# Optimization experiments

Measured on AMD Instinct MI355X. Metric: run time of the kernel, lower is better.

Reference implementation:

```python
import jax, jax.numpy as jnp
import numpy as np

S, N, E = 12, 16384, 262144        # timesteps, nodes, edges per timestep
DIN = DOUT = H = 128               # gcn in/out dim == lstm hidden (required by module)
B = 64                             # batch_size; N % B == 0


def setup_inputs() -> dict:
    key = jax.random.key(0)
    ks = jax.random.split(key, 10)
    return {
        "adj_indices": jax.random.randint(ks[0], (S, 2, E), 0, N, dtype=jnp.int32),
        "adj_values": jax.random.uniform(ks[1], (S, E), dtype=jnp.float32),
        "xs": jax.random.normal(ks[2], (S, N, DIN), dtype=jnp.float32),
        "gcn_weight": jax.random.normal(ks[3], (DIN, DOUT), dtype=jnp.float32) * 0.05,
        "gcn_bias": jnp.zeros((DOUT,), jnp.float32),
        "w_ih": jax.random.normal(ks[4], (4 * H, DOUT), dtype=jnp.float32) * 0.05,
        "w_hh": jax.random.normal(ks[5], (4 * H, H), dtype=jnp.float32) * 0.05,
        "b_ih": jnp.zeros((4 * H,), jnp.float32),
        "b_hh": jnp.zeros((4 * H,), jnp.float32),
        "h0": jax.random.normal(ks[6], (B, H), dtype=jnp.float32),
        "c0": jax.random.normal(ks[7], (B, H), dtype=jnp.float32),
    }


def reference(adj_indices, adj_values, xs, gcn_weight, gcn_bias,
              w_ih, w_hh, b_ih, b_hh, h0, c0):
    # --- GCN per timestep: relu(sparse_A @ (X @ W) + b) ---
    def gcn(idx, vals, x):
        support = x @ gcn_weight                      # [N, DOUT]
        msg = vals[:, None] * support[idx[1]]         # gather cols -> [E, DOUT]
        out = jax.ops.segment_sum(msg, idx[0], num_segments=N)  # scatter rows
        return jax.nn.relu(out + gcn_bias)

    cur = jax.vmap(gcn)(adj_indices, adj_values, xs)  # [S, N, DOUT]
    seq = cur.reshape(-1, B, DOUT)                    # [T=S*N/B, B, H]

    # --- single-layer LSTM (torch gate order: i, f, g, o) ---
    def step(carry, x_t):
        h, c = carry
        gates = x_t @ w_ih.T + b_ih + h @ w_hh.T + b_hh   # [B, 4H]
        i, f, g, o = jnp.split(gates, 4, axis=-1)
        c = jax.nn.sigmoid(f) * c + jax.nn.sigmoid(i) * jnp.tanh(g)
        h = jax.nn.sigmoid(o) * jnp.tanh(c)
        return (h, c), h

    _, hs = jax.lax.scan(step, (h0, c0), seq)         # [T, B, H]
    return hs
```

## Files before the change

kernel.cpp:

```cpp
#include <hip/hip_runtime.h>
#include <cstdint>
#include <cstddef>

#define SS 12
#define NN 16384
#define EE 262144
#define TT 3072

typedef _Float16 h2_t __attribute__((ext_vector_type(2)));
typedef _Float16 f16x8 __attribute__((ext_vector_type(8)));
typedef short bf16x8 __attribute__((ext_vector_type(8)));
typedef float floatx4 __attribute__((ext_vector_type(4)));
typedef unsigned short ushortx8 __attribute__((ext_vector_type(8)));

__device__ __forceinline__ float fast_sig(float x) {
    float e = __builtin_amdgcn_exp2f(-1.442695041f * x);
    return __builtin_amdgcn_rcpf(1.f + e);
}
__device__ __forceinline__ float fast_tanh(float x) {
    float e = __builtin_amdgcn_exp2f(2.885390082f * x);
    return 1.f - 2.f * __builtin_amdgcn_rcpf(e + 1.f);
}
__device__ __forceinline__ unsigned short f2bf(float f) {
    unsigned int x = __float_as_uint(f);
    unsigned int r = (x + 0x7FFFu + ((x >> 16) & 1u)) >> 16;
    return (unsigned short)r;
}
__device__ __forceinline__ float bf2f(unsigned short u) {
    return __uint_as_float(((unsigned int)u) << 16);
}

__global__ void k_zero(int* __restrict__ p) {
    p[blockIdx.x * 256 + threadIdx.x] = 0;
}

__global__ void k_count(const int* __restrict__ adj, int* __restrict__ counts) {
    int i = blockIdx.x * 256 + threadIdx.x;
    int t = i / EE, e = i - t * EE;
    int dst = adj[(size_t)t * 2 * EE + e];
    atomicAdd(&counts[t * NN + dst], 1);
}

__global__ void k_scan(const int* __restrict__ counts, int* __restrict__ offs,
                       int* __restrict__ cursor) {
    __shared__ int sums[1024];
    int t = blockIdx.x, tid = threadIdx.x;
    const int per = NN / 1024;
    int base = t * NN + tid * per;
    int local[16];
    int s = 0;
#pragma unroll
    for (int i = 0; i < per; i++) { local[i] = counts[base + i]; s += local[i]; }
    sums[tid] = s;
    __syncthreads();
    for (int off = 1; off < 1024; off <<= 1) {
        int v = (tid >= off) ? sums[tid - off] : 0;
        __syncthreads();
        sums[tid] += v;
        __syncthreads();
    }
    int run = sums[tid] - s;
#pragma unroll
    for (int i = 0; i < per; i++) { offs[base + i] = run; cursor[base + i] = run; run += local[i]; }
}

__global__ void k_scatter(const int* __restrict__ adj, const float* __restrict__ vals,
                          int* __restrict__ cursor, int2* __restrict__ edges) {
    int i = blockIdx.x * 256 + threadIdx.x;
    int t = i / EE, e = i - t * EE;
    int dst = adj[(size_t)t * 2 * EE + e];
    int src = adj[(size_t)t * 2 * EE + EE + e];
    float v = vals[(size_t)t * EE + e];
    int p = atomicAdd(&cursor[t * NN + dst], 1);
    edges[(size_t)t * EE + p] = make_int2(src, __float_as_int(v));
}

__global__ __launch_bounds__(256) void k_support(const float* __restrict__ xs,
                                                 const float* __restrict__ W,
                                                 unsigned short* __restrict__ sup) {
    __shared__ float Ash[64][128];
    __shared__ float Wsh[128][128];
    int tid = threadIdx.x;
    size_t rowbase = (size_t)blockIdx.x * 64;
    const float4* xa = (const float4*)(xs + rowbase * 128);
    float4* As = (float4*)&Ash[0][0];
#pragma unroll
    for (int q = 0; q < 8; q++) As[tid + q * 256] = xa[tid + q * 256];
    const float4* wg = (const float4*)W;
    float4* Ws = (float4*)&Wsh[0][0];
#pragma unroll
    for (int q = 0; q < 16; q++) Ws[tid + q * 256] = wg[tid + q * 256];
    __syncthreads();
    int jg = tid & 31, rg = tid >> 5;
    float acc[8][4];
#pragma unroll
    for (int i = 0; i < 8; i++)
#pragma unroll
        for (int j = 0; j < 4; j++) acc[i][j] = 0.f;
    for (int k4 = 0; k4 < 128; k4 += 4) {
        float4 a[8];
#pragma unroll
        for (int i = 0; i < 8; i++) a[i] = *(const float4*)&Ash[rg * 8 + i][k4];
#pragma unroll
        for (int kk = 0; kk < 4; kk++) {
            float4 wv = *(const float4*)&Wsh[k4 + kk][jg * 4];
#pragma unroll
            for (int i = 0; i < 8; i++) {
                float av = (kk == 0) ? a[i].x : (kk == 1) ? a[i].y : (kk == 2) ? a[i].z : a[i].w;
                acc[i][0] += av * wv.x; acc[i][1] += av * wv.y;
                acc[i][2] += av * wv.z; acc[i][3] += av * wv.w;
            }
        }
    }
#pragma unroll
    for (int i = 0; i < 8; i++) {
        ushort4 o;
        o.x = f2bf(acc[i][0]); o.y = f2bf(acc[i][1]);
        o.z = f2bf(acc[i][2]); o.w = f2bf(acc[i][3]);
        *(ushort4*)&sup[(rowbase + rg * 8 + i) * 128 + jg * 4] = o;
    }
}

__global__ __launch_bounds__(256) void k_gather(const int2* __restrict__ edges,
                         const int* __restrict__ offs,
                         const int* __restrict__ ends,
                         const unsigned short* __restrict__ sup,
                         const float* __restrict__ bias,
                         unsigned short* __restrict__ cur) {
    int bn = blockIdx.x * 4 + (threadIdx.x >> 6);
    bn = __builtin_amdgcn_readfirstlane(bn);
    int t = bn >> 14;
    int l = threadIdx.x & 63;
    int beg = offs[bn];
    int end = ends[bn];
    const unsigned short* supt = sup + (size_t)t * NN * 128;
    const int2* eg = edges + (size_t)t * EE;
    float acc0 = 0.f, acc1 = 0.f;
    int p = beg;
    for (; p + 3 < end; p += 4) {
        int2 e0 = eg[p], e1 = eg[p + 1], e2 = eg[p + 2], e3 = eg[p + 3];
        unsigned int u0 = *(const unsigned int*)&supt[(size_t)e0.x * 128 + 2 * l];
        unsigned int u1 = *(const unsigned int*)&supt[(size_t)e1.x * 128 + 2 * l];
        unsigned int u2 = *(const unsigned int*)&supt[(size_t)e2.x * 128 + 2 * l];
        unsigned int u3 = *(const unsigned int*)&supt[(size_t)e3.x * 128 + 2 * l];
        float w0 = __int_as_float(e0.y), w1 = __int_as_float(e1.y);
        float w2 = __int_as_float(e2.y), w3 = __int_as_float(e3.y);
        acc0 += w0 * bf2f((unsigned short)u0); acc1 += w0 * bf2f((unsigned short)(u0 >> 16));
        acc0 += w1 * bf2f((unsigned short)u1); acc1 += w1 * bf2f((unsigned short)(u1 >> 16));
        acc0 += w2 * bf2f((unsigned short)u2); acc1 += w2 * bf2f((unsigned short)(u2 >> 16));
        acc0 += w3 * bf2f((unsigned short)u3); acc1 += w3 * bf2f((unsigned short)(u3 >> 16));
    }
    for (; p < end; p++) {
        int2 e0 = eg[p];
        unsigned int u0 = *(const unsigned int*)&supt[(size_t)e0.x * 128 + 2 * l];
        float w0 = __int_as_float(e0.y);
        acc0 += w0 * bf2f((unsigned short)u0);
        acc1 += w0 * bf2f((unsigned short)(u0 >> 16));
    }
    float r0 = acc0 + bias[2 * l];
    float r1 = acc1 + bias[2 * l + 1];
    ushort2 o;
    o.x = f2bf(r0 > 0.f ? r0 : 0.f);
    o.y = f2bf(r1 > 0.f ? r1 : 0.f);
    *(ushort2*)&cur[(size_t)bn * 128 + 2 * l] = o;
}

__global__ __launch_bounds__(256) void k_xgates(const unsigned short* __restrict__ cur,
                                                const float* __restrict__ wih,
                                                const float* __restrict__ bih,
                                                const float* __restrict__ bhh,
                                                unsigned short* __restrict__ gx) {
    __shared__ __align__(16) unsigned short At[64][136];
    __shared__ __align__(16) unsigned short Bt[64][136];
    int tid = threadIdx.x;
    size_t rowbase = (size_t)blockIdx.x * 64;
    int gbase = blockIdx.y * 64;
#pragma unroll
    for (int q = 0; q < 4; q++) {
        int idx = tid + q * 256;
        int r = idx >> 4;
        int cc = (idx & 15) * 8;
        *(ushortx8*)&At[r][cc] = *(const ushortx8*)&cur[(rowbase + r) * 128 + cc];
    }
#pragma unroll
    for (int q = 0; q < 8; q++) {
        int idx = tid + q * 256;
        int r = idx >> 5;
        int c4 = (idx & 31) * 4;
        float4 v = *(const float4*)&wih[(size_t)(gbase + r) * 128 + c4];
        ushort4 o;
        o.x = f2bf(v.x); o.y = f2bf(v.y); o.z = f2bf(v.z); o.w = f2bf(v.w);
        *(ushort4*)&Bt[r][c4] = o;
    }
    __syncthreads();
    int wave = tid >> 6, lane = tid & 63;
    int m0 = wave * 16;
    int rin = lane & 15;
    int koff = (lane >> 4) * 8;
    floatx4 acc[4];
#pragma unroll
    for (int n = 0; n < 4; n++) acc[n] = (floatx4){0.f, 0.f, 0.f, 0.f};
#pragma unroll
    for (int kc = 0; kc < 4; kc++) {
        bf16x8 a = *(const bf16x8*)&At[m0 + rin][kc * 32 + koff];
#pragma unroll
        for (int n = 0; n < 4; n++) {
            bf16x8 b = *(const bf16x8*)&Bt[n * 16 + rin][kc * 32 + koff];
            acc[n] = __builtin_amdgcn_mfma_f32_16x16x32_bf16(a, b, acc[n], 0, 0, 0);
        }
    }
    int rq = (lane >> 4) * 4;
#pragma unroll
    for (int n = 0; n < 4; n++) {
        int gcol = gbase + n * 16 + rin;
        float bs = bih[gcol] + bhh[gcol];
        int slot = ((gcol & 127) << 2) | (gcol >> 7);
#pragma unroll
        for (int i = 0; i < 4; i++) {
            size_t row = rowbase + m0 + rq + i;
            gx[row * 512 + slot] = f2bf(acc[n][i] + bs);
        }
    }
}

__global__ __launch_bounds__(512, 2) void k_lstm(const unsigned short* __restrict__ gx,
                                                 const float* __restrict__ whh,
                                                 const float* __restrict__ h0,
                                                 const float* __restrict__ c0,
                                                 float* __restrict__ out) {
    __shared__ __align__(16) _Float16 hsh[2][128];
    int b = blockIdx.x, tid = threadIdx.x;
    int w = tid >> 6;
    int l = tid & 63;
    int col = l & 15;
    int kg = l >> 4;
    int j = w * 16 + col;

    f16x8 bw[4][4];
#pragma unroll
    for (int n = 0; n < 4; n++) {
        const float* rp = whh + (size_t)(n * 128 + j) * 128;
#pragma unroll
        for (int kt = 0; kt < 4; kt++) {
            int k0 = kt * 32 + kg * 8;
            float4 v0 = *(const float4*)(rp + k0);
            float4 v1 = *(const float4*)(rp + k0 + 4);
            f16x8 f;
            f[0] = (_Float16)v0.x; f[1] = (_Float16)v0.y;
            f[2] = (_Float16)v0.z; f[3] = (_Float16)v0.w;
            f[4] = (_Float16)v1.x; f[5] = (_Float16)v1.y;
            f[6] = (_Float16)v1.z; f[7] = (_Float16)v1.w;
            bw[n][kt] = f;
        }
    }
    float c = c0[(size_t)b * 128 + j];
    if (tid < 128) hsh[0][tid] = (_Float16)h0[(size_t)b * 128 + tid];
    __syncthreads();

    const unsigned short* gxb = gx + (size_t)b * 512 + 4 * j;
    uint2 rg0 = *(const uint2*)(gxb);
    uint2 rg1 = *(const uint2*)(gxb + 32768);
    uint2 rg2 = *(const uint2*)(gxb + 2 * (size_t)32768);

#define LSTM_STEP(T, RD, WR, QIDX)                                          \
    {                                                                       \
        f16x8 a0_ = *(const f16x8*)&hsh[RD][kg * 8];                        \
        f16x8 a1_ = *(const f16x8*)&hsh[RD][32 + kg * 8];                   \
        f16x8 a2_ = *(const f16x8*)&hsh[RD][64 + kg * 8];                   \
        f16x8 a3_ = *(const f16x8*)&hsh[RD][96 + kg * 8];                   \
        floatx4 ac0 = (floatx4){0.f, 0.f, 0.f, 0.f};                        \
        floatx4 ac1 = (floatx4){0.f, 0.f, 0.f, 0.f};                        \
        floatx4 ac2 = (floatx4){0.f, 0.f, 0.f, 0.f};                        \
        floatx4 ac3 = (floatx4){0.f, 0.f, 0.f, 0.f};                        \
        ac0 = __builtin_amdgcn_mfma_f32_16x16x32_f16(a0_, bw[0][0], ac0, 0, 0, 0); \
        ac1 = __builtin_amdgcn_mfma_f32_16x16x32_f16(a0_, bw[1][0], ac1, 0, 0, 0); \
        ac2 = __builtin_amdgcn_mfma_f32_16x16x32_f16(a0_, bw[2][0], ac2, 0, 0, 0); \
        ac3 = __builtin_amdgcn_mfma_f32_16x16x32_f16(a0_, bw[3][0], ac3, 0, 0, 0); \
        ac0 = __builtin_amdgcn_mfma_f32_16x16x32_f16(a1_, bw[0][1], ac0, 0, 0, 0); \
        ac1 = __builtin_amdgcn_mfma_f32_16x16x32_f16(a1_, bw[1][1], ac1, 0, 0, 0); \
        ac2 = __builtin_amdgcn_mfma_f32_16x16x32_f16(a1_, bw[2][1], ac2, 0, 0, 0); \
        ac3 = __builtin_amdgcn_mfma_f32_16x16x32_f16(a1_, bw[3][1], ac3, 0, 0, 0); \
        ac0 = __builtin_amdgcn_mfma_f32_16x16x32_f16(a2_, bw[0][2], ac0, 0, 0, 0); \
        ac1 = __builtin_amdgcn_mfma_f32_16x16x32_f16(a2_, bw[1][2], ac1, 0, 0, 0); \
        ac2 = __builtin_amdgcn_mfma_f32_16x16x32_f16(a2_, bw[2][2], ac2, 0, 0, 0); \
        ac3 = __builtin_amdgcn_mfma_f32_16x16x32_f16(a2_, bw[3][2], ac3, 0, 0, 0); \
        ac0 = __builtin_amdgcn_mfma_f32_16x16x32_f16(a3_, bw[0][3], ac0, 0, 0, 0); \
        ac1 = __builtin_amdgcn_mfma_f32_16x16x32_f16(a3_, bw[1][3], ac1, 0, 0, 0); \
        ac2 = __builtin_amdgcn_mfma_f32_16x16x32_f16(a3_, bw[2][3], ac2, 0, 0, 0); \
        ac3 = __builtin_amdgcn_mfma_f32_16x16x32_f16(a3_, bw[3][3], ac3, 0, 0, 0); \
        float ri_ = ac0[0] + bf2f((unsigned short)(rg0.x & 0xffffu));       \
        float rf_ = ac1[0] + bf2f((unsigned short)(rg0.x >> 16));           \
        float rg_ = ac2[0] + bf2f((unsigned short)(rg0.y & 0xffffu));       \
        float ro_ = ac3[0] + bf2f((unsigned short)(rg0.y >> 16));           \
        float ai_ = fast_sig(ri_);                                          \
        float af_ = fast_sig(rf_);                                          \
        float ag_ = fast_tanh(rg_);                                         \
        float ao_ = fast_sig(ro_);                                          \
        c = af_ * c + ai_ * ag_;                                            \
        float hn_ = ao_ * fast_tanh(c);                                     \
        hh8[QIDX] = hn_;                                                    \
        if (kg == 0) hsh[WR][j] = (_Float16)hn_;                            \
        rg0 = rg1; rg1 = rg2;                                               \
        {                                                                   \
            int tp_ = ((T) + 3 < TT) ? (T) + 3 : TT - 1;                    \
            rg2 = *(const uint2*)(gxb + (size_t)tp_ * 32768);               \
        }                                                                   \
        __syncthreads();                                                    \
    }

    for (int t8 = 0; t8 < TT; t8 += 8) {
        float hh8[8];
        LSTM_STEP(t8 + 0, 0, 1, 0);
        LSTM_STEP(t8 + 1, 1, 0, 1);
        LSTM_STEP(t8 + 2, 0, 1, 2);
        LSTM_STEP(t8 + 3, 1, 0, 3);
        LSTM_STEP(t8 + 4, 0, 1, 4);
        LSTM_STEP(t8 + 5, 1, 0, 5);
        LSTM_STEP(t8 + 6, 0, 1, 6);
        LSTM_STEP(t8 + 7, 1, 0, 7);
        if (kg == 0) {
#pragma unroll
            for (int qq = 0; qq < 8; qq++)
                out[((size_t)(t8 + qq) * 64 + b) * 128 + j] = hh8[qq];
        }
    }
#undef LSTM_STEP
}

extern "C" void kernel_launch(void* const* d_in, const int* in_sizes, int n_in,
                              void* d_out, int out_size, void* d_ws, size_t ws_size,
                              hipStream_t stream) {
    const int* adj    = (const int*)d_in[0];
    const float* vals = (const float*)d_in[1];
    const float* xs   = (const float*)d_in[2];
    const float* gw   = (const float*)d_in[3];
    const float* gb   = (const float*)d_in[4];
    const float* wih  = (const float*)d_in[5];
    const float* whh  = (const float*)d_in[6];
    const float* bih  = (const float*)d_in[7];
    const float* bhh  = (const float*)d_in[8];
    const float* h0   = (const float*)d_in[9];
    const float* c0   = (const float*)d_in[10];
    float* out = (float*)d_out;

    char* ws = (char*)d_ws;
    unsigned short* cur = (unsigned short*)(ws);
    unsigned short* gx  = (unsigned short*)(ws + 50331648);
    unsigned short* sup = (unsigned short*)(ws + 50331648);
    int* counts         = (int*)(ws + 100663296);
    int* offs           = (int*)(ws + 101449728);
    int* cursor         = (int*)(ws + 102236160);
    int2* edges         = (int2*)(ws + 103022592);

    k_zero<<<(SS * NN) / 256, 256, 0, stream>>>(counts);
    k_count<<<(SS * EE) / 256, 256, 0, stream>>>(adj, counts);
    k_scan<<<SS, 1024, 0, stream>>>(counts, offs, cursor);
    k_scatter<<<(SS * EE) / 256, 256, 0, stream>>>(adj, vals, cursor, edges);
    k_support<<<(SS * NN) / 64, 256, 0, stream>>>(xs, gw, sup);
    k_gather<<<(SS * NN) / 4, 256, 0, stream>>>(edges, offs, cursor, sup, gb, cur);
    k_xgates<<<dim3((SS * NN) / 64, 8), 256, 0, stream>>>(cur, wih, bih, bhh, gx);
    k_lstm<<<64, 512, 0, stream>>>(gx, whh, h0, c0, out);
}
```

Before: 2.291 ms.

## Split LSTM gate MFMA chains, fold bias into accumulators, loop xgates over gates

Each recurrent LSTM step now gives every gate two independent MFMA accumulator chains of depth 2 instead of one chain of depth 4. The x-gate preactivation is folded into the accumulator's initial value, and the sigmoid/tanh of finished gates is interleaved with the MFMAs of later gates. This is meant to shorten the serial per-step dependency path. The prefetch clamp is removed; the workspace is reordered so that reading past the end of gx lands in the cur buffer and stays valid memory. The x-gates kernel now keeps its A tile in LDS and loops over all 8 gate blocks, instead of launching a separate grid slice per gate block that reloads the same A tile.

```diff
diff --git a/kernel.cpp b/kernel.cpp
--- a/kernel.cpp
+++ b/kernel.cpp
@@ -174,7 +174,6 @@
     __shared__ __align__(16) unsigned short Bt[64][136];
     int tid = threadIdx.x;
     size_t rowbase = (size_t)blockIdx.x * 64;
-    int gbase = blockIdx.y * 64;
 #pragma unroll
     for (int q = 0; q < 4; q++) {
         int idx = tid + q * 256;
@@ -182,44 +181,48 @@
         int cc = (idx & 15) * 8;
         *(ushortx8*)&At[r][cc] = *(const ushortx8*)&cur[(rowbase + r) * 128 + cc];
     }
-#pragma unroll
-    for (int q = 0; q < 8; q++) {
-        int idx = tid + q * 256;
-        int r = idx >> 5;
-        int c4 = (idx & 31) * 4;
-        float4 v = *(const float4*)&wih[(size_t)(gbase + r) * 128 + c4];
-        ushort4 o;
-        o.x = f2bf(v.x); o.y = f2bf(v.y); o.z = f2bf(v.z); o.w = f2bf(v.w);
-        *(ushort4*)&Bt[r][c4] = o;
-    }
-    __syncthreads();
     int wave = tid >> 6, lane = tid & 63;
     int m0 = wave * 16;
     int rin = lane & 15;
     int koff = (lane >> 4) * 8;
-    floatx4 acc[4];
-#pragma unroll
-    for (int n = 0; n < 4; n++) acc[n] = (floatx4){0.f, 0.f, 0.f, 0.f};
-#pragma unroll
-    for (int kc = 0; kc < 4; kc++) {
-        bf16x8 a = *(const bf16x8*)&At[m0 + rin][kc * 32 + koff];
+    int rq = (lane >> 4) * 4;
+    for (int gb = 0; gb < 8; gb++) {
+        int gbase = gb * 64;
+#pragma unroll
+        for (int q = 0; q < 8; q++) {
+            int idx = tid + q * 256;
+            int r = idx >> 5;
+            int c4 = (idx & 31) * 4;
+            float4 v = *(const float4*)&wih[(size_t)(gbase + r) * 128 + c4];
+            ushort4 o;
+            o.x = f2bf(v.x); o.y = f2bf(v.y); o.z = f2bf(v.z); o.w = f2bf(v.w);
+            *(ushort4*)&Bt[r][c4] = o;
+        }
+        __syncthreads();
+        floatx4 acc[4];
+#pragma unroll
+        for (int n = 0; n < 4; n++) acc[n] = (floatx4){0.f, 0.f, 0.f, 0.f};
+#pragma unroll
+        for (int kc = 0; kc < 4; kc++) {
+            bf16x8 a = *(const bf16x8*)&At[m0 + rin][kc * 32 + koff];
+#pragma unroll
+            for (int n = 0; n < 4; n++) {
+                bf16x8 b = *(const bf16x8*)&Bt[n * 16 + rin][kc * 32 + koff];
+                acc[n] = __builtin_amdgcn_mfma_f32_16x16x32_bf16(a, b, acc[n], 0, 0, 0);
+            }
+        }
 #pragma unroll
         for (int n = 0; n < 4; n++) {
-            bf16x8 b = *(const bf16x8*)&Bt[n * 16 + rin][kc * 32 + koff];
-            acc[n] = __builtin_amdgcn_mfma_f32_16x16x32_bf16(a, b, acc[n], 0, 0, 0);
-        }
-    }
-    int rq = (lane >> 4) * 4;
-#pragma unroll
-    for (int n = 0; n < 4; n++) {
-        int gcol = gbase + n * 16 + rin;
-        float bs = bih[gcol] + bhh[gcol];
-        int slot = ((gcol & 127) << 2) | (gcol >> 7);
-#pragma unroll
-        for (int i = 0; i < 4; i++) {
-            size_t row = rowbase + m0 + rq + i;
-            gx[row * 512 + slot] = f2bf(acc[n][i] + bs);
-        }
+            int gcol = gbase + n * 16 + rin;
+            float bs = bih[gcol] + bhh[gcol];
+            int slot = ((gcol & 127) << 2) | (gcol >> 7);
+#pragma unroll
+            for (int i = 0; i < 4; i++) {
+                size_t row = rowbase + m0 + rq + i;
+                gx[row * 512 + slot] = f2bf(acc[n][i] + bs);
+            }
+        }
+        __syncthreads();
     }
 }
 
@@ -262,49 +265,45 @@
     uint2 rg1 = *(const uint2*)(gxb + 32768);
     uint2 rg2 = *(const uint2*)(gxb + 2 * (size_t)32768);
 
+#define MF(a, bfrag, acc) __builtin_amdgcn_mfma_f32_16x16x32_f16(a, bfrag, acc, 0, 0, 0)
+
 #define LSTM_STEP(T, RD, WR, QIDX)                                          \
     {                                                                       \
         f16x8 a0_ = *(const f16x8*)&hsh[RD][kg * 8];                        \
         f16x8 a1_ = *(const f16x8*)&hsh[RD][32 + kg * 8];                   \
         f16x8 a2_ = *(const f16x8*)&hsh[RD][64 + kg * 8];                   \
         f16x8 a3_ = *(const f16x8*)&hsh[RD][96 + kg * 8];                   \
-        floatx4 ac0 = (floatx4){0.f, 0.f, 0.f, 0.f};                        \
-        floatx4 ac1 = (floatx4){0.f, 0.f, 0.f, 0.f};                        \
-        floatx4 ac2 = (floatx4){0.f, 0.f, 0.f, 0.f};                        \
-        floatx4 ac3 = (floatx4){0.f, 0.f, 0.f, 0.f};                        \
-        ac0 = __builtin_amdgcn_mfma_f32_16x16x32_f16(a0_, bw[0][0], ac0, 0, 0, 0); \
-        ac1 = __builtin_amdgcn_mfma_f32_16x16x32_f16(a0_, bw[1][0], ac1, 0, 0, 0); \
-        ac2 = __builtin_amdgcn_mfma_f32_16x16x32_f16(a0_, bw[2][0], ac2, 0, 0, 0); \
-        ac3 = __builtin_amdgcn_mfma_f32_16x16x32_f16(a0_, bw[3][0], ac3, 0, 0, 0); \
-        ac0 = __builtin_amdgcn_mfma_f32_16x16x32_f16(a1_, bw[0][1], ac0, 0, 0, 0); \
-        ac1 = __builtin_amdgcn_mfma_f32_16x16x32_f16(a1_, bw[1][1], ac1, 0, 0, 0); \
-        ac2 = __builtin_amdgcn_mfma_f32_16x16x32_f16(a1_, bw[2][1], ac2, 0, 0, 0); \
-        ac3 = __builtin_amdgcn_mfma_f32_16x16x32_f16(a1_, bw[3][1], ac3, 0, 0, 0); \
-        ac0 = __builtin_amdgcn_mfma_f32_16x16x32_f16(a2_, bw[0][2], ac0, 0, 0, 0); \
-        ac1 = __builtin_amdgcn_mfma_f32_16x16x32_f16(a2_, bw[1][2], ac1, 0, 0, 0); \
-        ac2 = __builtin_amdgcn_mfma_f32_16x16x32_f16(a2_, bw[2][2], ac2, 0, 0, 0); \
-        ac3 = __builtin_amdgcn_mfma_f32_16x16x32_f16(a2_, bw[3][2], ac3, 0, 0, 0); \
-        ac0 = __builtin_amdgcn_mfma_f32_16x16x32_f16(a3_, bw[0][3], ac0, 0, 0, 0); \
-        ac1 = __builtin_amdgcn_mfma_f32_16x16x32_f16(a3_, bw[1][3], ac1, 0, 0, 0); \
-        ac2 = __builtin_amdgcn_mfma_f32_16x16x32_f16(a3_, bw[2][3], ac2, 0, 0, 0); \
-        ac3 = __builtin_amdgcn_mfma_f32_16x16x32_f16(a3_, bw[3][3], ac3, 0, 0, 0); \
-        float ri_ = ac0[0] + bf2f((unsigned short)(rg0.x & 0xffffu));       \
-        float rf_ = ac1[0] + bf2f((unsigned short)(rg0.x >> 16));           \
-        float rg_ = ac2[0] + bf2f((unsigned short)(rg0.y & 0xffffu));       \
-        float ro_ = ac3[0] + bf2f((unsigned short)(rg0.y >> 16));           \
-        float ai_ = fast_sig(ri_);                                          \
-        float af_ = fast_sig(rf_);                                          \
-        float ag_ = fast_tanh(rg_);                                         \
-        float ao_ = fast_sig(ro_);                                          \
+        float px0_ = bf2f((unsigned short)(rg0.x & 0xffffu));               \
+        float px1_ = bf2f((unsigned short)(rg0.x >> 16));                   \
+        float px2_ = bf2f((unsigned short)(rg0.y & 0xffffu));               \
+        float px3_ = bf2f((unsigned short)(rg0.y >> 16));                   \
+        floatx4 i0_ = (floatx4){px0_, 0.f, 0.f, 0.f};                       \
+        floatx4 i1_ = (floatx4){0.f, 0.f, 0.f, 0.f};                        \
+        i0_ = MF(a0_, bw[0][0], i0_); i1_ = MF(a1_, bw[0][1], i1_);         \
+        i0_ = MF(a2_, bw[0][2], i0_); i1_ = MF(a3_, bw[0][3], i1_);         \
+        floatx4 f0_ = (floatx4){px1_, 0.f, 0.f, 0.f};                       \
+        floatx4 f1_ = (floatx4){0.f, 0.f, 0.f, 0.f};                        \
+        f0_ = MF(a0_, bw[1][0], f0_); f1_ = MF(a1_, bw[1][1], f1_);         \
+        f0_ = MF(a2_, bw[1][2], f0_); f1_ = MF(a3_, bw[1][3], f1_);         \
+        float ai_ = fast_sig(i0_[0] + i1_[0]);                              \
+        floatx4 g0_ = (floatx4){px2_, 0.f, 0.f, 0.f};                       \
+        floatx4 g1_ = (floatx4){0.f, 0.f, 0.f, 0.f};                        \
+        g0_ = MF(a0_, bw[2][0], g0_); g1_ = MF(a1_, bw[2][1], g1_);         \
+        g0_ = MF(a2_, bw[2][2], g0_); g1_ = MF(a3_, bw[2][3], g1_);         \
+        float af_ = fast_sig(f0_[0] + f1_[0]);                              \
+        floatx4 o0_ = (floatx4){px3_, 0.f, 0.f, 0.f};                       \
+        floatx4 o1_ = (floatx4){0.f, 0.f, 0.f, 0.f};                        \
+        o0_ = MF(a0_, bw[3][0], o0_); o1_ = MF(a1_, bw[3][1], o1_);         \
+        o0_ = MF(a2_, bw[3][2], o0_); o1_ = MF(a3_, bw[3][3], o1_);         \
+        float ag_ = fast_tanh(g0_[0] + g1_[0]);                             \
         c = af_ * c + ai_ * ag_;                                            \
-        float hn_ = ao_ * fast_tanh(c);                                     \
+        float tc_ = fast_tanh(c);                                           \
+        float ao_ = fast_sig(o0_[0] + o1_[0]);                              \
+        float hn_ = ao_ * tc_;                                              \
         hh8[QIDX] = hn_;                                                    \
         if (kg == 0) hsh[WR][j] = (_Float16)hn_;                            \
         rg0 = rg1; rg1 = rg2;                                               \
-        {                                                                   \
-            int tp_ = ((T) + 3 < TT) ? (T) + 3 : TT - 1;                    \
-            rg2 = *(const uint2*)(gxb + (size_t)tp_ * 32768);               \
-        }                                                                   \
+        rg2 = *(const uint2*)(gxb + (size_t)((T) + 3) * 32768);             \
         __syncthreads();                                                    \
     }
 
@@ -325,6 +324,7 @@
         }
     }
 #undef LSTM_STEP
+#undef MF
 }
 
 extern "C" void kernel_launch(void* const* d_in, const int* in_sizes, int n_in,
@@ -344,13 +344,13 @@
     float* out = (float*)d_out;
 
     char* ws = (char*)d_ws;
-    unsigned short* cur = (unsigned short*)(ws);
-    unsigned short* gx  = (unsigned short*)(ws + 50331648);
-    unsigned short* sup = (unsigned short*)(ws + 50331648);
-    int* counts         = (int*)(ws + 100663296);
-    int* offs           = (int*)(ws + 101449728);
-    int* cursor         = (int*)(ws + 102236160);
-    int2* edges         = (int2*)(ws + 103022592);
+    unsigned short* gx  = (unsigned short*)(ws);
+    unsigned short* cur = (unsigned short*)(ws + 201326592);
+    unsigned short* sup = (unsigned short*)(ws);
+    int* counts         = (int*)(ws + 50331648);
+    int* offs           = (int*)(ws + 51118080);
+    int* cursor         = (int*)(ws + 51904512);
+    int2* edges         = (int2*)(ws + 52690944);
 
     k_zero<<<(SS * NN) / 256, 256, 0, stream>>>(counts);
     k_count<<<(SS * EE) / 256, 256, 0, stream>>>(adj, counts);
@@ -358,6 +358,6 @@
     k_scatter<<<(SS * EE) / 256, 256, 0, stream>>>(adj, vals, cursor, edges);
     k_support<<<(SS * NN) / 64, 256, 0, stream>>>(xs, gw, sup);
     k_gather<<<(SS * NN) / 4, 256, 0, stream>>>(edges, offs, cursor, sup, gb, cur);
-    k_xgates<<<dim3((SS * NN) / 64, 8), 256, 0, stream>>>(cur, wih, bih, bhh, gx);
+    k_xgates<<<(SS * NN) / 64, 256, 0, stream>>>(cur, wih, bih, bhh, gx);
     k_lstm<<<64, 512, 0, stream>>>(gx, whh, h0, c0, out);
 }
```

New measurement: 2.335 ms. About the same (+1.9%).
